# Performance work log

Hardware: AMD Instinct MI355X
Metric: run time of the kernel (lower is better)

Reference implementation:

```python
import jax, jax.numpy as jnp
import numpy as np

VOCAB = 11322
EMB = 300
HID = 512
B, K, T = 64, 100, 20
NUM_QT = 84
NUM_ANS = 30000


def _lstm_layer(x, lens, w_ih, w_hh, b_ih, b_hh):
    """x: [N, T, in], lens: [N]. PyTorch gate order i,f,g,o.
    Returns (outputs [N, T, H], final hidden at t == len-1 [N, H])."""
    N = x.shape[0]
    H = w_hh.shape[1]
    x_t = jnp.swapaxes(x, 0, 1)  # [T, N, in]
    ts = jnp.arange(x.shape[1])

    def step(carry, inp):
        h, c = carry
        xt, t = inp
        gates = xt @ w_ih.T + h @ w_hh.T + (b_ih + b_hh)  # [N, 4H]
        i, f, g, o = jnp.split(gates, 4, axis=-1)
        c_new = jax.nn.sigmoid(f) * c + jax.nn.sigmoid(i) * jnp.tanh(g)
        h_new = jax.nn.sigmoid(o) * jnp.tanh(c_new)
        mask = (t < lens)[:, None]  # freeze state past each seq's length
        h = jnp.where(mask, h_new, h)
        c = jnp.where(mask, c_new, c)
        return (h, c), h

    init = (jnp.zeros((N, H), x.dtype), jnp.zeros((N, H), x.dtype))
    (h_fin, _), ys = jax.lax.scan(step, init, (x_t, ts))
    return jnp.swapaxes(ys, 0, 1), h_fin


def setup_inputs() -> dict:
    key = jax.random.key(0)
    ks = jax.random.split(key, 16)
    s = 1.0 / np.sqrt(HID)
    W_embed = jax.random.normal(ks[0], (VOCAB, EMB), jnp.float32) * 0.02
    W_embed = W_embed.at[0].set(0.0)  # padding_idx=0
    inp = {
        'encoder_output': jax.random.normal(ks[1], (B, HID), jnp.float32),
        'opt': jax.random.randint(ks[2], (B, K, T), 0, VOCAB),
        'opt_len': jax.random.randint(ks[3], (B, K), 1, T + 1),
        'qt_idx': jax.random.randint(ks[4], (B,), 0, NUM_QT),
        'opt_idx': jax.random.randint(ks[5], (B, K), 0, NUM_ANS),
        'W_embed': W_embed,
        'w_ih0': jax.random.uniform(ks[6], (4 * HID, EMB), jnp.float32, -s, s),
        'w_hh0': jax.random.uniform(ks[7], (4 * HID, HID), jnp.float32, -s, s),
        'b_ih0': jax.random.uniform(ks[8], (4 * HID,), jnp.float32, -s, s),
        'b_hh0': jax.random.uniform(ks[9], (4 * HID,), jnp.float32, -s, s),
        'w_ih1': jax.random.uniform(ks[10], (4 * HID, HID), jnp.float32, -s, s),
        'w_hh1': jax.random.uniform(ks[11], (4 * HID, HID), jnp.float32, -s, s),
        'b_ih1': jax.random.uniform(ks[12], (4 * HID,), jnp.float32, -s, s),
        'b_hh1': jax.random.uniform(ks[13], (4 * HID,), jnp.float32, -s, s),
        'relevance': jax.random.uniform(ks[14], (NUM_QT, NUM_ANS)) < 0.02,
    }
    return inp


def reference(encoder_output, opt, opt_len, qt_idx, opt_idx, W_embed,
              w_ih0, w_hh0, b_ih0, b_hh0, w_ih1, w_hh1, b_ih1, b_hh1,
              relevance):
    bsz, num_opt, max_len = opt.shape
    options = opt.reshape(-1, max_len)            # [B*K, T]
    lens = opt_len.reshape(-1)                    # [B*K]
    emb = W_embed[options] * (options != 0)[..., None].astype(W_embed.dtype)
    ys1, _ = _lstm_layer(emb, lens, w_ih0, w_hh0, b_ih0, b_hh0)
    _, h2 = _lstm_layer(ys1, lens, w_ih1, w_hh1, b_ih1, b_hh1)
    options_feat = h2.reshape(bsz, num_opt, HID)
    scores = jnp.einsum('bkh,bh->bk', options_feat, encoder_output)
    # vectorized replacement of the per-sample dict-lookup loop
    qt_score = relevance[qt_idx[:, None], opt_idx].astype(scores.dtype)
    return scores, qt_score
```

## Files before the change

### kernel.cpp

```cpp
#include <hip/hip_runtime.h>

#define NSEQ 6400
#define TMAX 20
#define EMB 300
#define EMBP 320
#define HID 512
#define KL0 832
#define KL1 1024
#define NQT 84
#define NANS 30000
#define RELN (NQT * NANS)

typedef __bf16 bf16x8 __attribute__((ext_vector_type(8)));
typedef float f32x4 __attribute__((ext_vector_type(4)));
typedef unsigned short u16;

__device__ __forceinline__ u16 f2bf(float f) {
  union { float f; unsigned int i; } v; v.f = f;
  unsigned int r = v.i + 0x7fffu + ((v.i >> 16) & 1u);
  return (u16)(r >> 16);
}

__global__ __launch_bounds__(320) void embed_kernel(
    const int* __restrict__ opt, const float* __restrict__ Wemb, u16* __restrict__ embT) {
  int n = blockIdx.x;
  int e = threadIdx.x;
#pragma unroll 4
  for (int t = 0; t < TMAX; ++t) {
    int tok = opt[n * TMAX + t];
    float v = 0.f;
    if (e < EMB && tok != 0) v = Wemb[(size_t)tok * EMB + e];
    embT[((size_t)t * NSEQ + n) * EMBP + e] = f2bf(v);
  }
}

__global__ void prep_w0(const float* __restrict__ wih, const float* __restrict__ whh,
                        u16* __restrict__ W) {
  for (int idx = blockIdx.x * blockDim.x + threadIdx.x; idx < 2048 * KL0;
       idx += gridDim.x * blockDim.x) {
    int o = idx / KL0, c = idx % KL0;
    float v;
    if (c < EMB) v = wih[o * EMB + c];
    else if (c < EMBP) v = 0.f;
    else v = whh[o * HID + (c - EMBP)];
    W[idx] = f2bf(v);
  }
}
__global__ void prep_w1(const float* __restrict__ wih, const float* __restrict__ whh,
                        u16* __restrict__ W) {
  for (int idx = blockIdx.x * blockDim.x + threadIdx.x; idx < 2048 * KL1;
       idx += gridDim.x * blockDim.x) {
    int o = idx / KL1, c = idx % KL1;
    float v = (c < HID) ? wih[o * HID + c] : whh[o * HID + (c - HID)];
    W[idx] = f2bf(v);
  }
}
__global__ void prep_bias(const float* __restrict__ a, const float* __restrict__ b,
                          float* __restrict__ o) {
  int i = blockIdx.x * blockDim.x + threadIdx.x;
  if (i < 2048) o[i] = a[i] + b[i];
}

__global__ __launch_bounds__(256) void lstm_step(
    const u16* __restrict__ segA0, int strideA0, int K0,
    const u16* __restrict__ segA1,
    const u16* __restrict__ Wcat, int Ktot, int nK,
    const float* __restrict__ biasc,
    u16* __restrict__ h_new, float* __restrict__ c_state,
    const float* __restrict__ hf_old, float* __restrict__ hf_new,
    const int* __restrict__ lens, int t) {
  __shared__ __align__(16) u16 Atile[3][128 * 32];
  __shared__ __align__(16) u16 Btile[3][128 * 32];
  const int tid = threadIdx.x;
  const int wave = tid >> 6, lane = tid & 63;
  const int l15 = lane & 15, l4 = lane >> 4;
  const int wr = wave >> 1, wc = wave & 1;

  const int orig = blockIdx.x;
  const int nid = (orig & 7) * 100 + (orig >> 3);
  const int rowBlk = (nid >> 4) * 128;
  const int hb = (nid & 15) * 32;

  const bool isA = wave < 2;
  const int ld0 = (wave & 1) * 4;
  int offg[4], offg1[4];
#pragma unroll
  for (int i = 0; i < 4; ++i) {
    int lrow = (ld0 + i) * 16 + (lane >> 2);
    int srcslot = (lane & 3) ^ ((lrow >> 1) & 3);
    if (isA) {
      offg[i]  = (rowBlk + lrow) * strideA0 + srcslot * 8;
      offg1[i] = (rowBlk + lrow) * HID + srcslot * 8;
    } else {
      int g = lrow >> 5, h = lrow & 31;
      offg[i]  = (g * HID + hb + h) * Ktot + srcslot * 8;
      offg1[i] = 0;
    }
  }

  auto stage = [&](int sel, int ks) {
    const int kbase = ks * 32;
    if (isA) {
      const bool s1 = kbase >= K0;
      const u16* base = s1 ? (segA1 + (kbase - K0)) : (segA0 + kbase);
      const int* off = s1 ? offg1 : offg;
#pragma unroll
      for (int i = 0; i < 4; ++i)
        __builtin_amdgcn_global_load_lds(
            (const __attribute__((address_space(1))) void*)(base + off[i]),
            (__attribute__((address_space(3))) void*)(&Atile[sel][(ld0 + i) * 512]),
            16, 0, 0);
    } else {
#pragma unroll
      for (int i = 0; i < 4; ++i)
        __builtin_amdgcn_global_load_lds(
            (const __attribute__((address_space(1))) void*)(Wcat + offg[i] + kbase),
            (__attribute__((address_space(3))) void*)(&Btile[sel][(ld0 + i) * 512]),
            16, 0, 0);
    }
  };

  f32x4 acc[4][4] = {};
  const int kx = (l4 ^ ((l15 >> 1) & 3)) * 8;

  auto compute = [&](int sel) {
    bf16x8 a[4], b[4];
#pragma unroll
    for (int m = 0; m < 4; ++m)
      a[m] = *(const bf16x8*)(&Atile[sel][(wr * 64 + m * 16 + l15) * 32 + kx]);
#pragma unroll
    for (int g = 0; g < 4; ++g)
      b[g] = *(const bf16x8*)(&Btile[sel][(g * 32 + wc * 16 + l15) * 32 + kx]);
    __builtin_amdgcn_s_setprio(1);
#pragma unroll
    for (int m = 0; m < 4; ++m)
#pragma unroll
      for (int g = 0; g < 4; ++g)
        acc[m][g] = __builtin_amdgcn_mfma_f32_16x16x32_bf16(a[m], b[g], acc[m][g], 0, 0, 0);
    __builtin_amdgcn_s_setprio(0);
  };

  stage(0, 0);
  stage(1, 1);
  int sel = 0, pre = 2;
  for (int ks = 0; ks < nK; ++ks) {
    if (ks + 2 < nK) {
      stage(pre, ks + 2);
      if (++pre == 3) pre = 0;
      asm volatile("s_waitcnt vmcnt(8)" ::: "memory");
    } else if (ks + 1 < nK) {
      asm volatile("s_waitcnt vmcnt(4)" ::: "memory");
    } else {
      asm volatile("s_waitcnt vmcnt(0)" ::: "memory");
    }
    __builtin_amdgcn_s_barrier();
    compute(sel);
    if (++sel == 3) sel = 0;
    if (ks + 1 < nK) __builtin_amdgcn_s_barrier();
  }

  const int u = hb + wc * 16 + l15;
  const float bi = biasc[u], bff = biasc[512 + u], bg = biasc[1024 + u], bo = biasc[1536 + u];
#pragma unroll
  for (int m = 0; m < 4; ++m) {
    const int rbase = rowBlk + wr * 64 + m * 16 + l4 * 4;
    const size_t cmi = (size_t)u * NSEQ + rbase;
    f32x4 co4 = *(const f32x4*)(c_state + cmi);
    int4 ln4 = *(const int4*)(lens + rbase);
    f32x4 ho4;
    if (hf_new) ho4 = *(const f32x4*)(hf_old + cmi);
    f32x4 cn4, hn4;
    u16 hstore[4];
#pragma unroll
    for (int jj = 0; jj < 4; ++jj) {
      const int r = rbase + jj;
      float ip = acc[m][0][jj] + bi;
      float fp = acc[m][1][jj] + bff;
      float gp = acc[m][2][jj] + bg;
      float op = acc[m][3][jj] + bo;
      float co = co4[jj];
      float si = 1.f / (1.f + __expf(-ip));
      float sf = 1.f / (1.f + __expf(-fp));
      float so = 1.f / (1.f + __expf(-op));
      float tg = tanhf(gp);
      float cn = sf * co + si * tg;
      float hn = so * tanhf(cn);
      int len = (jj == 0) ? ln4.x : (jj == 1) ? ln4.y : (jj == 2) ? ln4.z : ln4.w;
      bool act = t < len;
      cn4[jj] = act ? cn : co;
      hstore[jj] = act ? f2bf(hn) : segA1[(size_t)r * HID + u];
      if (hf_new) hn4[jj] = act ? hn : ho4[jj];
    }
    *(f32x4*)(c_state + cmi) = cn4;
    if (hf_new) *(f32x4*)(hf_new + cmi) = hn4;
#pragma unroll
    for (int jj = 0; jj < 4; ++jj)
      h_new[(size_t)(rbase + jj) * HID + u] = hstore[jj];
  }
}

__global__ __launch_bounds__(256) void scores_kernel(
    const float* __restrict__ h2cm, const float* __restrict__ enc, float* __restrict__ out) {
  int n = (blockIdx.x >> 1) * 256 + threadIdx.x;
  int uh = (blockIdx.x & 1) * 256;
  const float* ep = enc + (n / 100) * HID + uh;
  float s = 0.f;
#pragma unroll 8
  for (int u = 0; u < 256; ++u) s += h2cm[(size_t)(uh + u) * NSEQ + n] * ep[u];
  atomicAdd(&out[n], s);
}

__global__ void detect_kernel(const unsigned char* __restrict__ rel, int* __restrict__ flags) {
  int a = 0, bb = 0, z = 0;
  for (int i = blockIdx.x * blockDim.x + threadIdx.x; i < RELN; i += gridDim.x * blockDim.x) {
    if (rel[i]) {
      if (i & 3) a = 1; else z = 1;
      if (i & 4) bb = 1;
    }
  }
  if (a) atomicOr(&flags[0], 1);
  if (bb) atomicOr(&flags[1], 1);
  if (z) atomicOr(&flags[2], 1);
}

__global__ void qt_kernel(const void* __restrict__ rel, const int* __restrict__ qt_idx,
                          const int* __restrict__ opt_idx, const int* __restrict__ flags,
                          float* __restrict__ out) {
  int n = blockIdx.x * blockDim.x + threadIdx.x;
  if (n >= NSEQ) return;
  long long idx = (long long)qt_idx[n / 100] * NANS + opt_idx[n];
  int fa = flags[0], fb = flags[1], fz = flags[2];
  bool hit;
  if (fa && fz)       hit = ((const unsigned char*)rel)[idx] != 0;
  else if (fa)        hit = ((const float*)rel)[idx] != 0.f;
  else if (fb)        hit = ((const int*)rel)[idx] != 0;
  else                hit = ((const long long*)rel)[idx] != 0;
  out[NSEQ + n] = hit ? 1.f : 0.f;
}

extern "C" void kernel_launch(void* const* d_in, const int* in_sizes, int n_in,
                              void* d_out, int out_size, void* d_ws, size_t ws_size,
                              hipStream_t stream) {
  (void)in_sizes; (void)n_in; (void)out_size; (void)ws_size;
  const float* enc    = (const float*)d_in[0];
  const int*   opt    = (const int*)d_in[1];
  const int*   optlen = (const int*)d_in[2];
  const int*   qtidx  = (const int*)d_in[3];
  const int*   optidx = (const int*)d_in[4];
  const float* Wemb   = (const float*)d_in[5];
  const float* wih0   = (const float*)d_in[6];
  const float* whh0   = (const float*)d_in[7];
  const float* bih0   = (const float*)d_in[8];
  const float* bhh0   = (const float*)d_in[9];
  const float* wih1   = (const float*)d_in[10];
  const float* whh1   = (const float*)d_in[11];
  const float* bih1   = (const float*)d_in[12];
  const float* bhh1   = (const float*)d_in[13];
  const void*  rel    = d_in[14];
  float* out = (float*)d_out;

  char* ws = (char*)d_ws;
  size_t off = 0;
  auto alloc = [&](size_t bytes) -> void* {
    void* p = (void*)(ws + off);
    off += (bytes + 255) & ~(size_t)255;
    return p;
  };
  u16* embT   = (u16*)alloc((size_t)TMAX * NSEQ * EMBP * 2);
  u16* W0     = (u16*)alloc((size_t)2048 * KL0 * 2);
  u16* W1     = (u16*)alloc((size_t)2048 * KL1 * 2);
  float* bc0  = (float*)alloc(2048 * 4);
  float* bc1  = (float*)alloc(2048 * 4);
  u16* h0b[2] = { (u16*)alloc((size_t)NSEQ * HID * 2), (u16*)alloc((size_t)NSEQ * HID * 2) };
  u16* h1b[2] = { (u16*)alloc((size_t)NSEQ * HID * 2), (u16*)alloc((size_t)NSEQ * HID * 2) };
  float* c0   = (float*)alloc((size_t)NSEQ * HID * 4);
  float* c1   = (float*)alloc((size_t)NSEQ * HID * 4);
  float* hf[2] = { (float*)alloc((size_t)NSEQ * HID * 4), (float*)alloc((size_t)NSEQ * HID * 4) };
  int* flags  = (int*)alloc(16);

  hipMemsetAsync(h0b[0], 0, (size_t)NSEQ * HID * 2, stream);
  hipMemsetAsync(h1b[0], 0, (size_t)NSEQ * HID * 2, stream);
  hipMemsetAsync(c0, 0, (size_t)NSEQ * HID * 4, stream);
  hipMemsetAsync(c1, 0, (size_t)NSEQ * HID * 4, stream);
  hipMemsetAsync(hf[0], 0, (size_t)NSEQ * HID * 4, stream);
  hipMemsetAsync(flags, 0, 16, stream);
  hipMemsetAsync(out, 0, (size_t)NSEQ * 4, stream);

  embed_kernel<<<NSEQ, EMBP, 0, stream>>>(opt, Wemb, embT);
  prep_w0<<<512, 256, 0, stream>>>(wih0, whh0, W0);
  prep_w1<<<512, 256, 0, stream>>>(wih1, whh1, W1);
  prep_bias<<<8, 256, 0, stream>>>(bih0, bhh0, bc0);
  prep_bias<<<8, 256, 0, stream>>>(bih1, bhh1, bc1);
  detect_kernel<<<256, 256, 0, stream>>>((const unsigned char*)rel, flags);

  for (int t = 0; t < TMAX; ++t) {
    int cur = t & 1, nxt = cur ^ 1;
    lstm_step<<<800, 256, 0, stream>>>(
        embT + (size_t)t * NSEQ * EMBP, EMBP, EMBP,
        h0b[cur], W0, KL0, KL0 / 32, bc0,
        h0b[nxt], c0, nullptr, nullptr, optlen, t);
    lstm_step<<<800, 256, 0, stream>>>(
        h0b[nxt], HID, HID,
        h1b[cur], W1, KL1, KL1 / 32, bc1,
        h1b[nxt], c1, hf[cur], hf[nxt], optlen, t);
  }

  scores_kernel<<<50, 256, 0, stream>>>(hf[0], enc, out);
  qt_kernel<<<(NSEQ + 255) / 256, 256, 0, stream>>>(rel, qtidx, optidx, flags, out);
}
```

Baseline: 2.228 ms.

## Use eight waves per LSTM step block with half the rows per wave

Doubles the workgroup to 512 threads (8 waves) and splits the 128x128 output tile so each wave computes 32 rows by 64 gate columns instead of 64x64. Every wave now issues one A load and one B load per k-step instead of four of one kind, and the waitcnt thresholds are adjusted to match. The aim is more latency hiding and shorter per-wave MFMA chains in this latency-bound recurrent step. In exchange each wave reuses its B fragments across fewer A rows, so LDS read traffic per MFMA goes up, and the larger block may limit how many blocks fit on a CU.

```diff
diff --git a/kernel.cpp b/kernel.cpp
--- a/kernel.cpp
+++ b/kernel.cpp
@@ -61,7 +61,7 @@
   if (i < 2048) o[i] = a[i] + b[i];
 }
 
-__global__ __launch_bounds__(256) void lstm_step(
+__global__ __launch_bounds__(512) void lstm_step(
     const u16* __restrict__ segA0, int strideA0, int K0,
     const u16* __restrict__ segA1,
     const u16* __restrict__ Wcat, int Ktot, int nK,
@@ -81,59 +81,42 @@
   const int rowBlk = (nid >> 4) * 128;
   const int hb = (nid & 15) * 32;
 
-  const bool isA = wave < 2;
-  const int ld0 = (wave & 1) * 4;
-  int offg[4], offg1[4];
-#pragma unroll
-  for (int i = 0; i < 4; ++i) {
-    int lrow = (ld0 + i) * 16 + (lane >> 2);
-    int srcslot = (lane & 3) ^ ((lrow >> 1) & 3);
-    if (isA) {
-      offg[i]  = (rowBlk + lrow) * strideA0 + srcslot * 8;
-      offg1[i] = (rowBlk + lrow) * HID + srcslot * 8;
-    } else {
-      int g = lrow >> 5, h = lrow & 31;
-      offg[i]  = (g * HID + hb + h) * Ktot + srcslot * 8;
-      offg1[i] = 0;
-    }
-  }
+  const int jhi = lane >> 2;
+  const int lrow = wave * 16 + jhi;
+  const int srcslot = (lane & 3) ^ ((lrow >> 1) & 3);
+  const int offA0 = (rowBlk + lrow) * strideA0 + srcslot * 8;
+  const int offA1 = (rowBlk + lrow) * HID + srcslot * 8;
+  const int gB = lrow >> 5, hB = lrow & 31;
+  const int offB = (gB * HID + hb + hB) * Ktot + srcslot * 8;
 
   auto stage = [&](int sel, int ks) {
     const int kbase = ks * 32;
-    if (isA) {
-      const bool s1 = kbase >= K0;
-      const u16* base = s1 ? (segA1 + (kbase - K0)) : (segA0 + kbase);
-      const int* off = s1 ? offg1 : offg;
-#pragma unroll
-      for (int i = 0; i < 4; ++i)
-        __builtin_amdgcn_global_load_lds(
-            (const __attribute__((address_space(1))) void*)(base + off[i]),
-            (__attribute__((address_space(3))) void*)(&Atile[sel][(ld0 + i) * 512]),
-            16, 0, 0);
-    } else {
-#pragma unroll
-      for (int i = 0; i < 4; ++i)
-        __builtin_amdgcn_global_load_lds(
-            (const __attribute__((address_space(1))) void*)(Wcat + offg[i] + kbase),
-            (__attribute__((address_space(3))) void*)(&Btile[sel][(ld0 + i) * 512]),
-            16, 0, 0);
-    }
+    const bool s1 = kbase >= K0;
+    const u16* aPtr = s1 ? (segA1 + (kbase - K0) + offA1) : (segA0 + kbase + offA0);
+    __builtin_amdgcn_global_load_lds(
+        (const __attribute__((address_space(1))) void*)aPtr,
+        (__attribute__((address_space(3))) void*)(&Atile[sel][wave * 512]),
+        16, 0, 0);
+    __builtin_amdgcn_global_load_lds(
+        (const __attribute__((address_space(1))) void*)(Wcat + offB + kbase),
+        (__attribute__((address_space(3))) void*)(&Btile[sel][wave * 512]),
+        16, 0, 0);
   };
 
-  f32x4 acc[4][4] = {};
+  f32x4 acc[2][4] = {};
   const int kx = (l4 ^ ((l15 >> 1) & 3)) * 8;
 
   auto compute = [&](int sel) {
-    bf16x8 a[4], b[4];
-#pragma unroll
-    for (int m = 0; m < 4; ++m)
-      a[m] = *(const bf16x8*)(&Atile[sel][(wr * 64 + m * 16 + l15) * 32 + kx]);
+    bf16x8 a[2], b[4];
+#pragma unroll
+    for (int m = 0; m < 2; ++m)
+      a[m] = *(const bf16x8*)(&Atile[sel][(wr * 32 + m * 16 + l15) * 32 + kx]);
 #pragma unroll
     for (int g = 0; g < 4; ++g)
       b[g] = *(const bf16x8*)(&Btile[sel][(g * 32 + wc * 16 + l15) * 32 + kx]);
     __builtin_amdgcn_s_setprio(1);
 #pragma unroll
-    for (int m = 0; m < 4; ++m)
+    for (int m = 0; m < 2; ++m)
 #pragma unroll
       for (int g = 0; g < 4; ++g)
         acc[m][g] = __builtin_amdgcn_mfma_f32_16x16x32_bf16(a[m], b[g], acc[m][g], 0, 0, 0);
@@ -147,9 +130,9 @@
     if (ks + 2 < nK) {
       stage(pre, ks + 2);
       if (++pre == 3) pre = 0;
-      asm volatile("s_waitcnt vmcnt(8)" ::: "memory");
+      asm volatile("s_waitcnt vmcnt(4)" ::: "memory");
     } else if (ks + 1 < nK) {
-      asm volatile("s_waitcnt vmcnt(4)" ::: "memory");
+      asm volatile("s_waitcnt vmcnt(2)" ::: "memory");
     } else {
       asm volatile("s_waitcnt vmcnt(0)" ::: "memory");
     }
@@ -162,8 +145,8 @@
   const int u = hb + wc * 16 + l15;
   const float bi = biasc[u], bff = biasc[512 + u], bg = biasc[1024 + u], bo = biasc[1536 + u];
 #pragma unroll
-  for (int m = 0; m < 4; ++m) {
-    const int rbase = rowBlk + wr * 64 + m * 16 + l4 * 4;
+  for (int m = 0; m < 2; ++m) {
+    const int rbase = rowBlk + wr * 32 + m * 16 + l4 * 4;
     const size_t cmi = (size_t)u * NSEQ + rbase;
     f32x4 co4 = *(const f32x4*)(c_state + cmi);
     int4 ln4 = *(const int4*)(lens + rbase);
@@ -295,11 +278,11 @@
 
   for (int t = 0; t < TMAX; ++t) {
     int cur = t & 1, nxt = cur ^ 1;
-    lstm_step<<<800, 256, 0, stream>>>(
+    lstm_step<<<800, 512, 0, stream>>>(
         embT + (size_t)t * NSEQ * EMBP, EMBP, EMBP,
         h0b[cur], W0, KL0, KL0 / 32, bc0,
         h0b[nxt], c0, nullptr, nullptr, optlen, t);
-    lstm_step<<<800, 256, 0, stream>>>(
+    lstm_step<<<800, 512, 0, stream>>>(
         h0b[nxt], HID, HID,
         h1b[cur], W1, KL1, KL1 / 32, bc1,
         h1b[nxt], c1, hf[cur], hf[nxt], optlen, t);
```

Result: slower. 2.323 ms (+4.2%).
